# Kernel tuning notes

Hardware: AMD Instinct MI355X
Metric: run time of the kernel (lower is better)

Reference implementation:

```python
import jax, jax.numpy as jnp
import numpy as np

B, S, I, Q, H = 512, 196, 2048, 1024, 512


def _attn(X, g, wx, bx, wg, bg, wh, bh):
    # X: (B, S, F); g: (B, G) or None
    feat = jnp.einsum('bsf,fh->bsh', X, wx) + bx
    if g is not None:
        feat = feat + (g @ wg + bg)[:, None, :]
    h = jnp.tanh(feat)
    score = jnp.einsum('bsh,h->bs', h, wh) + bh  # (B, S)
    a = jax.nn.softmax(score, axis=1)
    return jnp.einsum('bs,bsf->bf', a, X)


def setup_inputs() -> dict:
    key = jax.random.key(0)
    ks = jax.random.split(key, 16)
    sc = lambda n: 1.0 / np.sqrt(n)
    d = {
        'ques_feat': jax.random.normal(ks[0], (B, Q), jnp.float32),
        'img_feat': jax.random.normal(ks[1], (B, S, I), jnp.float32),
        # attn1: X=ques (Q), no guidance
        'w1x': jax.random.uniform(ks[2], (Q, H), jnp.float32, -sc(Q), sc(Q)),
        'b1x': jnp.zeros((H,), jnp.float32),
        'w1h': jax.random.uniform(ks[3], (H,), jnp.float32, -sc(H), sc(H)),
        'b1h': jnp.zeros((), jnp.float32),
        # attn2: X=img (I), guidance=ques (Q)
        'w2x': jax.random.uniform(ks[4], (I, H), jnp.float32, -sc(I), sc(I)),
        'b2x': jnp.zeros((H,), jnp.float32),
        'w2g': jax.random.uniform(ks[5], (Q, H), jnp.float32, -sc(Q), sc(Q)),
        'b2g': jnp.zeros((H,), jnp.float32),
        'w2h': jax.random.uniform(ks[6], (H,), jnp.float32, -sc(H), sc(H)),
        'b2h': jnp.zeros((), jnp.float32),
        # attn3: X=ques (Q), guidance=img-attended (I)
        'w3x': jax.random.uniform(ks[7], (Q, H), jnp.float32, -sc(Q), sc(Q)),
        'b3x': jnp.zeros((H,), jnp.float32),
        'w3g': jax.random.uniform(ks[8], (I, H), jnp.float32, -sc(I), sc(I)),
        'b3g': jnp.zeros((H,), jnp.float32),
        'w3h': jax.random.uniform(ks[9], (H,), jnp.float32, -sc(H), sc(H)),
        'b3h': jnp.zeros((), jnp.float32),
    }
    return d


def reference(ques_feat, img_feat, w1x, b1x, w1h, b1h, w2x, b2x, w2g, b2g,
              w2h, b2h, w3x, b3x, w3g, b3g, w3h, b3h):
    q = ques_feat[:, None, :]  # (B, 1, Q)
    ques_self = _attn(q, None, w1x, b1x, None, None, w1h, b1h)          # (B, Q)
    img_attn = _attn(img_feat, ques_self, w2x, b2x, w2g, b2g, w2h, b2h)  # (B, I)
    ques_attn = _attn(q, img_attn, w3x, b3x, w3g, b3g, w3h, b3h)         # (B, Q)
    return (ques_attn, img_attn)
```

## Files before the change

kernel.cpp:

```cpp
#include <hip/hip_runtime.h>
#include <hip/hip_bf16.h>
#include <cstdint>


typedef __attribute__((ext_vector_type(8))) short bf16x8;
typedef __attribute__((ext_vector_type(4))) float f32x4;

typedef __attribute__((address_space(1))) const unsigned int as1_uint;
typedef __attribute__((address_space(3))) unsigned int as3_uint;

__device__ inline unsigned short f2bf(float f) {
    union { float f; unsigned u; } v; v.f = f;
    unsigned u = v.u;
    u += 0x7FFFu + ((u >> 16) & 1u);
    return (unsigned short)(u >> 16);
}

__device__ inline unsigned pk2(float lo, float hi) {
    __hip_bfloat162 h = __float22bfloat162_rn(make_float2(lo, hi));
    return *reinterpret_cast<unsigned*>(&h);
}

__device__ inline bf16x8 cvt8(uint4 lo, uint4 hi) {
    union { uint4 q; float f[4]; } a, b; a.q = lo; b.q = hi;
    union { unsigned u[4]; bf16x8 v; } r;
    r.u[0] = pk2(a.f[0], a.f[1]); r.u[1] = pk2(a.f[2], a.f[3]);
    r.u[2] = pk2(b.f[0], b.f[1]); r.u[3] = pk2(b.f[2], b.f[3]);
    return r.v;
}

__global__ void k_copy(const float* __restrict__ src, float* __restrict__ dst) {
    int i = blockIdx.x * blockDim.x + threadIdx.x;
    reinterpret_cast<float4*>(dst)[i] = reinterpret_cast<const float4*>(src)[i];
}

__global__ void k_pack_w(const float* __restrict__ w, unsigned short* __restrict__ wtf) {
    int kblk = blockIdx.x >> 5;
    int nblk = blockIdx.x & 31;
    int t = threadIdx.x;
    int kc8 = t >> 4, col = t & 15;
    const float* src = w + (size_t)(kblk * 64 + kc8 * 8) * 512 + nblk * 16 + col;
    unsigned short* dst = wtf + (size_t)(kblk * 32 + nblk) * 1024 + kc8 * 128 + col * 8;
    unsigned short tmp[8];
    #pragma unroll
    for (int j = 0; j < 8; ++j) tmp[j] = f2bf(src[(size_t)j * 512]);
    *reinterpret_cast<uint4*>(dst) = *reinterpret_cast<const uint4*>(tmp);
}

__global__ void k_cconst(const float* __restrict__ qf, const float* __restrict__ w2g,
                         const float* __restrict__ b2g, const float* __restrict__ b2x,
                         float* __restrict__ cc) {
    __shared__ float qls[2][1024];
    int b0 = blockIdx.x * 2;
    int t = threadIdx.x;
    #pragma unroll
    for (int j = 0; j < 2; ++j) {
        int idx = j * 256 + t;
        int bb = idx >> 8, c4 = idx & 255;
        float4 v = reinterpret_cast<const float4*>(qf + (size_t)(b0 + bb) * 1024)[c4];
        qls[bb][c4 * 4 + 0] = v.x; qls[bb][c4 * 4 + 1] = v.y;
        qls[bb][c4 * 4 + 2] = v.z; qls[bb][c4 * 4 + 3] = v.w;
    }
    __syncthreads();
    float a00 = 0.f, a01 = 0.f, a10 = 0.f, a11 = 0.f;
    #pragma unroll 8
    for (int q = 0; q < 1024; ++q) {
        float w0 = w2g[q * 512 + t];
        float w1 = w2g[q * 512 + 256 + t];
        float q0 = qls[0][q], q1 = qls[1][q];
        a00 += q0 * w0; a01 += q0 * w1;
        a10 += q1 * w0; a11 += q1 * w1;
    }
    float c0 = b2g[t] + b2x[t];
    float c1 = b2g[t + 256] + b2x[t + 256];
    cc[(size_t)b0 * 512 + t] = a00 + c0;
    cc[(size_t)b0 * 512 + t + 256] = a01 + c1;
    cc[(size_t)(b0 + 1) * 512 + t] = a10 + c0;
    cc[(size_t)(b0 + 1) * 512 + t + 256] = a11 + c1;
}

#define NSTEP 32

__global__ __launch_bounds__(512, 4) void k_scores(
    const float* __restrict__ X, const unsigned short* __restrict__ WTf,
    const float* __restrict__ cc, const float* __restrict__ w2h,
    float* __restrict__ scores)
{
    __shared__ __align__(16) char Ab[4][16384];
    __shared__ float slds[64];

    int tid = threadIdx.x;
    int wave = tid >> 6, lane = tid & 63;
    int l15 = lane & 15, l4 = lane >> 4;
    int r0 = blockIdx.x * 64;

    int srow = tid >> 4, spc = tid & 15;
    const char* xsrc = reinterpret_cast<const char*>(X + (size_t)(r0 + srow) * 2048)
                       + ((spc ^ (srow & 15)) << 4);
    const char* xsrc2 = xsrc + (size_t)32 * 8192;
    char* ldsw = &Ab[0][0] + wave * 1024;

    const unsigned short* wb0 = WTf + (size_t)wave * 4096 + l4 * 128 + l15 * 8;

    const char* abase = &Ab[0][0];
    int off00 = l15 * 256 + (((l4 * 2 + 0) ^ l15) << 4);
    int off01 = l15 * 256 + (((l4 * 2 + 1) ^ l15) << 4);
    int off10 = l15 * 256 + (((8 + l4 * 2 + 0) ^ l15) << 4);
    int off11 = l15 * 256 + (((8 + l4 * 2 + 1) ^ l15) << 4);

    if (tid < 64) slds[tid] = 0.0f;

    f32x4 acc[4][4];
    #pragma unroll
    for (int m = 0; m < 4; ++m)
        #pragma unroll
        for (int n = 0; n < 4; ++n) acc[m][n] = (f32x4){0.f, 0.f, 0.f, 0.f};

    bf16x8 brA[4], brB[4];

    #define GLOAD2(bufofs, step) do { \
        __builtin_amdgcn_global_load_lds((as1_uint*)(xsrc + (step) * 256), \
            (as3_uint*)(ldsw + (bufofs)), 16, 0, 2); \
        __builtin_amdgcn_global_load_lds((as1_uint*)(xsrc2 + (step) * 256), \
            (as3_uint*)(ldsw + (bufofs) + 8192), 16, 0, 2); } while (0)

    #define BLOAD(dst, t, kh) do { \
        const unsigned short* bp = wb0 + (size_t)(t) * 32768 + (kh) * 512; \
        dst[0] = *reinterpret_cast<const bf16x8*>(bp); \
        dst[1] = *reinterpret_cast<const bf16x8*>(bp + 1024); \
        dst[2] = *reinterpret_cast<const bf16x8*>(bp + 2048); \
        dst[3] = *reinterpret_cast<const bf16x8*>(bp + 3072); } while (0)

    #define MF(br, bufofs, offL, offH) do { \
        __builtin_amdgcn_s_setprio(1); \
        _Pragma("unroll") \
        for (int m = 0; m < 4; ++m) { \
            uint4 lo = *reinterpret_cast<const uint4*>(abase + (bufofs) + m * 4096 + (offL)); \
            uint4 hi = *reinterpret_cast<const uint4*>(abase + (bufofs) + m * 4096 + (offH)); \
            bf16x8 af = cvt8(lo, hi); \
            _Pragma("unroll") \
            for (int n = 0; n < 4; ++n) \
                acc[m][n] = __builtin_amdgcn_mfma_f32_16x16x32_bf16(af, br[n], acc[m][n], 0, 0, 0); \
        } \
        __builtin_amdgcn_s_setprio(0); } while (0)

    #define SBAR __builtin_amdgcn_sched_barrier(0)

    GLOAD2(0, 0);
    GLOAD2(16384, 1);
    GLOAD2(32768, 2);
    BLOAD(brA, 0, 0);
    asm volatile("s_waitcnt vmcnt(12)" ::: "memory");
    __builtin_amdgcn_s_barrier();

    #pragma unroll 1
    for (int t = 0; t < NSTEP; ++t) {
        int bufofs = (t & 3) * 16384;
        BLOAD(brB, t, 1);
        MF(brA, bufofs, off00, off01);
        if (t + 1 < NSTEP) BLOAD(brA, t + 1, 0);
        MF(brB, bufofs, off10, off11);
        SBAR;
        if (t + 3 < NSTEP) GLOAD2(((t + 3) & 3) * 16384, t + 3);
        SBAR;
        __builtin_amdgcn_s_barrier();
    }

    asm volatile("" ::: "memory");

    int b0 = r0 / 196;
    int sbreak = (b0 + 1) * 196 - r0;
    int b1 = b0 + 1; if (b1 > 511) b1 = 511;
    float cch0[4], cch1[4], whv[4];
    #pragma unroll
    for (int n = 0; n < 4; ++n) {
        int h = wave * 64 + n * 16 + l15;
        cch0[n] = cc[(size_t)b0 * 512 + h];
        cch1[n] = cc[(size_t)b1 * 512 + h];
        whv[n] = w2h[h];
    }
    #pragma unroll
    for (int m = 0; m < 4; ++m) {
        #pragma unroll
        for (int i = 0; i < 4; ++i) {
            int row = m * 16 + l4 * 4 + i;
            float p = 0.0f;
            #pragma unroll
            for (int n = 0; n < 4; ++n) {
                float x = acc[m][n][i] + ((row < sbreak) ? cch0[n] : cch1[n]);
                float th = 1.0f - 2.0f / (__expf(2.0f * x) + 1.0f);
                p += th * whv[n];
            }
            p += __shfl_xor(p, 1);
            p += __shfl_xor(p, 2);
            p += __shfl_xor(p, 4);
            p += __shfl_xor(p, 8);
            if (l15 == 0) atomicAdd(&slds[row], p);
        }
    }
    __syncthreads();
    if (tid < 64) scores[(size_t)r0 + tid] = slds[tid];
}

__global__ void k_softmax(float* sc) {
    int b = blockIdx.x, t = threadIdx.x;
    __shared__ float red[8];
    float v = (t < 196) ? sc[(size_t)b * 196 + t] : -3.0e38f;
    float m = v;
    for (int o = 32; o > 0; o >>= 1) m = fmaxf(m, __shfl_xor(m, o));
    if ((t & 63) == 0) red[t >> 6] = m;
    __syncthreads();
    m = fmaxf(fmaxf(red[0], red[1]), fmaxf(red[2], red[3]));
    float e = (t < 196) ? __expf(v - m) : 0.0f;
    float s = e;
    for (int o = 32; o > 0; o >>= 1) s += __shfl_xor(s, o);
    if ((t & 63) == 0) red[4 + (t >> 6)] = s;
    __syncthreads();
    float tot = red[4] + red[5] + red[6] + red[7];
    if (t < 196) sc[(size_t)b * 196 + t] = e / tot;
}

__global__ void k_wsum(const float* __restrict__ X, const float* __restrict__ a,
                       float* __restrict__ out1) {
    __shared__ float als[196];
    int b = blockIdx.x >> 1;
    int fh = (blockIdx.x & 1) * 1024;
    int t = threadIdx.x;
    if (t < 196) als[t] = a[(size_t)b * 196 + t];
    __syncthreads();
    int f = fh + t * 4;
    const float* Xb = X + (size_t)b * 196 * 2048 + f;
    float4 acc = {0.f, 0.f, 0.f, 0.f};
    #pragma unroll 4
    for (int s = 0; s < 196; ++s) {
        float4 x = *reinterpret_cast<const float4*>(Xb + (size_t)s * 2048);
        float w = als[s];
        acc.x += w * x.x; acc.y += w * x.y; acc.z += w * x.z; acc.w += w * x.w;
    }
    *reinterpret_cast<float4*>(out1 + (size_t)b * 2048 + f) = acc;
}

extern "C" void kernel_launch(void* const* d_in, const int* in_sizes, int n_in,
                              void* d_out, int out_size, void* d_ws, size_t ws_size,
                              hipStream_t stream) {
    const float* qf  = (const float*)d_in[0];
    const float* X   = (const float*)d_in[1];
    const float* w2x = (const float*)d_in[6];
    const float* b2x = (const float*)d_in[7];
    const float* w2g = (const float*)d_in[8];
    const float* b2g = (const float*)d_in[9];
    const float* w2h = (const float*)d_in[10];

    float* out0 = (float*)d_out;
    float* out1 = out0 + 512 * 1024;

    unsigned short* WTf = (unsigned short*)d_ws;
    float* cc = (float*)((char*)d_ws + (size_t)(2u << 20));
    float* sc = (float*)((char*)d_ws + (size_t)(3u << 20));

    k_copy<<<512, 256, 0, stream>>>(qf, out0);
    k_pack_w<<<1024, 128, 0, stream>>>(w2x, WTf);
    k_cconst<<<256, 256, 0, stream>>>(qf, w2g, b2g, b2x, cc);
    k_scores<<<1568, 512, 0, stream>>>(X, WTf, cc, w2h, sc);
    k_softmax<<<512, 256, 0, stream>>>(sc);
    k_wsum<<<1024, 256, 0, stream>>>(X, sc, out1);
}
```

Before: 531.1 us.

## Widen score K-tile and emit bf16 X copy for weighted sum

```diff
diff --git a/kernel.cpp b/kernel.cpp
--- a/kernel.cpp
+++ b/kernel.cpp
@@ -21,12 +21,23 @@
     return *reinterpret_cast<unsigned*>(&h);
 }
 
+__device__ inline unsigned pkq(unsigned a, unsigned b) {
+    union { unsigned u; float f; } x, y; x.u = a; y.u = b;
+    return pk2(x.f, y.f);
+}
+
 __device__ inline bf16x8 cvt8(uint4 lo, uint4 hi) {
-    union { uint4 q; float f[4]; } a, b; a.q = lo; b.q = hi;
     union { unsigned u[4]; bf16x8 v; } r;
-    r.u[0] = pk2(a.f[0], a.f[1]); r.u[1] = pk2(a.f[2], a.f[3]);
-    r.u[2] = pk2(b.f[0], b.f[1]); r.u[3] = pk2(b.f[2], b.f[3]);
+    r.u[0] = pkq(lo.x, lo.y); r.u[1] = pkq(lo.z, lo.w);
+    r.u[2] = pkq(hi.x, hi.y); r.u[3] = pkq(hi.z, hi.w);
     return r.v;
+}
+
+__device__ inline float bfhi(unsigned u) {
+    union { unsigned u; float f; } v; v.u = u & 0xFFFF0000u; return v.f;
+}
+__device__ inline float bflo(unsigned u) {
+    union { unsigned u; float f; } v; v.u = u << 16; return v.f;
 }
 
 __global__ void k_copy(const float* __restrict__ src, float* __restrict__ dst) {
@@ -79,14 +90,15 @@
     cc[(size_t)(b0 + 1) * 512 + t + 256] = a11 + c1;
 }
 
-#define NSTEP 32
-
-__global__ __launch_bounds__(512, 4) void k_scores(
+#define NSTEP 16
+
+template<int DOX>
+__global__ __launch_bounds__(512, 2) void k_scores_t(
     const float* __restrict__ X, const unsigned short* __restrict__ WTf,
     const float* __restrict__ cc, const float* __restrict__ w2h,
-    float* __restrict__ scores)
+    float* __restrict__ scores, unsigned short* __restrict__ xbf)
 {
-    __shared__ __align__(16) char Ab[4][16384];
+    __shared__ __align__(16) char Ab[4][32768];
     __shared__ float slds[64];
 
     int tid = threadIdx.x;
@@ -94,19 +106,25 @@
     int l15 = lane & 15, l4 = lane >> 4;
     int r0 = blockIdx.x * 64;
 
-    int srow = tid >> 4, spc = tid & 15;
-    const char* xsrc = reinterpret_cast<const char*>(X + (size_t)(r0 + srow) * 2048)
-                       + ((spc ^ (srow & 15)) << 4);
-    const char* xsrc2 = xsrc + (size_t)32 * 8192;
+    int srow = tid >> 5;
+    int spc = tid & 31;
+    int g0 = (spc ^ srow) << 4;
+    int g1 = (spc ^ (srow + 16)) << 4;
+    const char* xs0 = reinterpret_cast<const char*>(X + (size_t)(r0 + srow) * 2048) + g0;
+    const char* xs1 = reinterpret_cast<const char*>(X + (size_t)(r0 + srow + 16) * 2048) + g1;
+    const char* xs2 = reinterpret_cast<const char*>(X + (size_t)(r0 + srow + 32) * 2048) + g0;
+    const char* xs3 = reinterpret_cast<const char*>(X + (size_t)(r0 + srow + 48) * 2048) + g1;
     char* ldsw = &Ab[0][0] + wave * 1024;
 
     const unsigned short* wb0 = WTf + (size_t)wave * 4096 + l4 * 128 + l15 * 8;
 
     const char* abase = &Ab[0][0];
-    int off00 = l15 * 256 + (((l4 * 2 + 0) ^ l15) << 4);
-    int off01 = l15 * 256 + (((l4 * 2 + 1) ^ l15) << 4);
-    int off10 = l15 * 256 + (((8 + l4 * 2 + 0) ^ l15) << 4);
-    int off11 = l15 * 256 + (((8 + l4 * 2 + 1) ^ l15) << 4);
+    int q0v = ((l4 * 2 + 0) ^ l15) << 4;
+    int q1v = ((l4 * 2 + 1) ^ l15) << 4;
+    int voff0 = l15 * 512 + q0v;
+    int voff1 = l15 * 512 + q1v;
+
+    char* xd = reinterpret_cast<char*>(xbf) + (size_t)blockIdx.x * 262144 + tid * 32;
 
     if (tid < 64) slds[tid] = 0.0f;
 
@@ -116,27 +134,31 @@
         #pragma unroll
         for (int n = 0; n < 4; ++n) acc[m][n] = (f32x4){0.f, 0.f, 0.f, 0.f};
 
-    bf16x8 brA[4], brB[4];
-
-    #define GLOAD2(bufofs, step) do { \
-        __builtin_amdgcn_global_load_lds((as1_uint*)(xsrc + (step) * 256), \
-            (as3_uint*)(ldsw + (bufofs)), 16, 0, 2); \
-        __builtin_amdgcn_global_load_lds((as1_uint*)(xsrc2 + (step) * 256), \
-            (as3_uint*)(ldsw + (bufofs) + 8192), 16, 0, 2); } while (0)
+    bf16x8 brA[4], brB[4], brC[4];
+
+    #define GLL(src, dst) __builtin_amdgcn_global_load_lds( \
+        (as1_uint*)(src), (as3_uint*)(dst), 16, 0, 2)
+
+    #define GLOAD4(bufofs, step) do { \
+        GLL(xs0 + (size_t)(step) * 512, ldsw + (bufofs)); \
+        GLL(xs1 + (size_t)(step) * 512, ldsw + (bufofs) + 8192); \
+        GLL(xs2 + (size_t)(step) * 512, ldsw + (bufofs) + 16384); \
+        GLL(xs3 + (size_t)(step) * 512, ldsw + (bufofs) + 24576); } while (0)
 
     #define BLOAD(dst, t, kh) do { \
-        const unsigned short* bp = wb0 + (size_t)(t) * 32768 + (kh) * 512; \
+        const unsigned short* bp = wb0 + (size_t)(2 * (t) + ((kh) >> 1)) * 32768 + ((kh) & 1) * 512; \
         dst[0] = *reinterpret_cast<const bf16x8*>(bp); \
         dst[1] = *reinterpret_cast<const bf16x8*>(bp + 1024); \
         dst[2] = *reinterpret_cast<const bf16x8*>(bp + 2048); \
         dst[3] = *reinterpret_cast<const bf16x8*>(bp + 3072); } while (0)
 
-    #define MF(br, bufofs, offL, offH) do { \
+    #define MF(br, bufofs, kh) do { \
         __builtin_amdgcn_s_setprio(1); \
         _Pragma("unroll") \
         for (int m = 0; m < 4; ++m) { \
-            uint4 lo = *reinterpret_cast<const uint4*>(abase + (bufofs) + m * 4096 + (offL)); \
-            uint4 hi = *reinterpret_cast<const uint4*>(abase + (bufofs) + m * 4096 + (offH)); \
+            int cst = ((kh) * 128) ^ ((m & 1) * 256); \
+            uint4 lo = *reinterpret_cast<const uint4*>(abase + (bufofs) + m * 8192 + (voff0 ^ cst)); \
+            uint4 hi = *reinterpret_cast<const uint4*>(abase + (bufofs) + m * 8192 + (voff1 ^ cst)); \
             bf16x8 af = cvt8(lo, hi); \
             _Pragma("unroll") \
             for (int n = 0; n < 4; ++n) \
@@ -144,27 +166,44 @@
         } \
         __builtin_amdgcn_s_setprio(0); } while (0)
 
-    #define SBAR __builtin_amdgcn_sched_barrier(0)
-
-    GLOAD2(0, 0);
-    GLOAD2(16384, 1);
-    GLOAD2(32768, 2);
+    #define STORE_TILE(bufofs, t) do { if (DOX) { \
+        const uint4* sp = reinterpret_cast<const uint4*>(abase + (bufofs) + tid * 64); \
+        uint4 s0 = sp[0], s1 = sp[1], s2 = sp[2], s3 = sp[3]; \
+        uint4 o0, o1; \
+        o0.x = pkq(s0.x, s0.y); o0.y = pkq(s0.z, s0.w); \
+        o0.z = pkq(s1.x, s1.y); o0.w = pkq(s1.z, s1.w); \
+        o1.x = pkq(s2.x, s2.y); o1.y = pkq(s2.z, s2.w); \
+        o1.z = pkq(s3.x, s3.y); o1.w = pkq(s3.z, s3.w); \
+        *reinterpret_cast<uint4*>(xd + (size_t)(t) * 16384) = o0; \
+        *reinterpret_cast<uint4*>(xd + (size_t)(t) * 16384 + 16) = o1; } } while (0)
+
+    #define STEP(T, SA, SB, SC, LAST) do { \
+        const int bo_ = ((T) & 3) * 32768; \
+        if ((T) + 3 < NSTEP) GLOAD4((((T) + 3) & 3) * 32768, (T) + 3); \
+        MF(SA, bo_, 0); BLOAD(SA, (T), 3); \
+        MF(SB, bo_, 1); if (!(LAST)) BLOAD(SB, (T) + 1, 0); \
+        MF(SC, bo_, 2); if (!(LAST)) BLOAD(SC, (T) + 1, 1); \
+        MF(SA, bo_, 3); if (!(LAST)) BLOAD(SA, (T) + 1, 2); \
+        STORE_TILE(bo_, T); \
+        __builtin_amdgcn_sched_barrier(0); \
+        __builtin_amdgcn_s_barrier(); } while (0)
+
+    GLOAD4(0, 0);
+    GLOAD4(32768, 1);
+    GLOAD4(65536, 2);
     BLOAD(brA, 0, 0);
-    asm volatile("s_waitcnt vmcnt(12)" ::: "memory");
+    BLOAD(brB, 0, 1);
+    BLOAD(brC, 0, 2);
+    asm volatile("s_waitcnt vmcnt(20)" ::: "memory");
     __builtin_amdgcn_s_barrier();
 
     #pragma unroll 1
-    for (int t = 0; t < NSTEP; ++t) {
-        int bufofs = (t & 3) * 16384;
-        BLOAD(brB, t, 1);
-        MF(brA, bufofs, off00, off01);
-        if (t + 1 < NSTEP) BLOAD(brA, t + 1, 0);
-        MF(brB, bufofs, off10, off11);
-        SBAR;
-        if (t + 3 < NSTEP) GLOAD2(((t + 3) & 3) * 16384, t + 3);
-        SBAR;
-        __builtin_amdgcn_s_barrier();
-    }
+    for (int T = 0; T < 15; T += 3) {
+        STEP(T,     brA, brB, brC, 0);
+        STEP(T + 1, brB, brC, brA, 0);
+        STEP(T + 2, brC, brA, brB, 0);
+    }
+    STEP(15, brA, brB, brC, 1);
 
     asm volatile("" ::: "memory");
 
@@ -220,6 +259,36 @@
     if (t < 196) sc[(size_t)b * 196 + t] = e / tot;
 }
 
+__global__ __launch_bounds__(256) void k_wsum_bf(const unsigned short* __restrict__ Xbf,
+                                                 const float* __restrict__ a,
+                                                 float* __restrict__ out1) {
+    __shared__ float als[196];
+    int b = blockIdx.x >> 1;
+    int half = blockIdx.x & 1;
+    int t = threadIdx.x;
+    if (t < 196) als[t] = a[(size_t)b * 196 + t];
+    __syncthreads();
+    int f = half * 1024 + t * 4;
+    int cg = f >> 2;
+    int step = cg >> 5;
+    int gcolin = cg & 31;
+    const char* xb = reinterpret_cast<const char*>(Xbf);
+    float a0 = 0.f, a1 = 0.f, a2 = 0.f, a3 = 0.f;
+    int r = b * 196;
+    #pragma unroll 4
+    for (int s = 0; s < 196; ++s, ++r) {
+        int tile = r >> 6, row = r & 63;
+        size_t byte = (size_t)tile * 262144 + (size_t)step * 16384
+                      + (size_t)(row * 32 + (gcolin ^ (row & 31))) * 8;
+        uint2 v = *reinterpret_cast<const uint2*>(xb + byte);
+        float w = als[s];
+        a0 += w * bflo(v.x); a1 += w * bfhi(v.x);
+        a2 += w * bflo(v.y); a3 += w * bfhi(v.y);
+    }
+    float4 o = {a0, a1, a2, a3};
+    *reinterpret_cast<float4*>(out1 + (size_t)b * 2048 + f) = o;
+}
+
 __global__ void k_wsum(const float* __restrict__ X, const float* __restrict__ a,
                        float* __restrict__ out1) {
     __shared__ float als[196];
@@ -257,11 +326,20 @@
     unsigned short* WTf = (unsigned short*)d_ws;
     float* cc = (float*)((char*)d_ws + (size_t)(2u << 20));
     float* sc = (float*)((char*)d_ws + (size_t)(3u << 20));
+    unsigned short* xbf = (unsigned short*)((char*)d_ws + (size_t)(4u << 20));
+    const size_t XBF_BYTES = (size_t)1568 * 262144;
+    int big = (ws_size >= (size_t)(4u << 20) + XBF_BYTES) ? 1 : 0;
 
     k_copy<<<512, 256, 0, stream>>>(qf, out0);
     k_pack_w<<<1024, 128, 0, stream>>>(w2x, WTf);
     k_cconst<<<256, 256, 0, stream>>>(qf, w2g, b2g, b2x, cc);
-    k_scores<<<1568, 512, 0, stream>>>(X, WTf, cc, w2h, sc);
-    k_softmax<<<512, 256, 0, stream>>>(sc);
-    k_wsum<<<1024, 256, 0, stream>>>(X, sc, out1);
-}
+    if (big) {
+        k_scores_t<1><<<1568, 512, 0, stream>>>(X, WTf, cc, w2h, sc, xbf);
+        k_softmax<<<512, 256, 0, stream>>>(sc);
+        k_wsum_bf<<<1024, 256, 0, stream>>>(xbf, sc, out1);
+    } else {
+        k_scores_t<0><<<1568, 512, 0, stream>>>(X, WTf, cc, w2h, sc, xbf);
+        k_softmax<<<512, 256, 0, stream>>>(sc);
+        k_wsum<<<1024, 256, 0, stream>>>(X, sc, out1);
+    }
+}
```

New measurement: 553.3 us. 1.04x slower.

## Emit bf16 copy of image tiles from scoring kernel for weighted sum

Applied to the files above, without the earlier changes.

```diff
diff --git a/kernel.cpp b/kernel.cpp
--- a/kernel.cpp
+++ b/kernel.cpp
@@ -21,12 +21,23 @@
     return *reinterpret_cast<unsigned*>(&h);
 }
 
+__device__ inline unsigned pkq(unsigned a, unsigned b) {
+    union { unsigned u; float f; } x, y; x.u = a; y.u = b;
+    return pk2(x.f, y.f);
+}
+
 __device__ inline bf16x8 cvt8(uint4 lo, uint4 hi) {
-    union { uint4 q; float f[4]; } a, b; a.q = lo; b.q = hi;
     union { unsigned u[4]; bf16x8 v; } r;
-    r.u[0] = pk2(a.f[0], a.f[1]); r.u[1] = pk2(a.f[2], a.f[3]);
-    r.u[2] = pk2(b.f[0], b.f[1]); r.u[3] = pk2(b.f[2], b.f[3]);
+    r.u[0] = pkq(lo.x, lo.y); r.u[1] = pkq(lo.z, lo.w);
+    r.u[2] = pkq(hi.x, hi.y); r.u[3] = pkq(hi.z, hi.w);
     return r.v;
+}
+
+__device__ inline float bfhi(unsigned u) {
+    union { unsigned u; float f; } v; v.u = u & 0xFFFF0000u; return v.f;
+}
+__device__ inline float bflo(unsigned u) {
+    union { unsigned u; float f; } v; v.u = u << 16; return v.f;
 }
 
 __global__ void k_copy(const float* __restrict__ src, float* __restrict__ dst) {
@@ -81,10 +92,11 @@
 
 #define NSTEP 32
 
-__global__ __launch_bounds__(512, 4) void k_scores(
+template<int DOX>
+__global__ __launch_bounds__(512, 4) void k_scores_t(
     const float* __restrict__ X, const unsigned short* __restrict__ WTf,
     const float* __restrict__ cc, const float* __restrict__ w2h,
-    float* __restrict__ scores)
+    float* __restrict__ scores, unsigned short* __restrict__ xbf)
 {
     __shared__ __align__(16) char Ab[4][16384];
     __shared__ float slds[64];
@@ -107,6 +119,8 @@
     int off01 = l15 * 256 + (((l4 * 2 + 1) ^ l15) << 4);
     int off10 = l15 * 256 + (((8 + l4 * 2 + 0) ^ l15) << 4);
     int off11 = l15 * 256 + (((8 + l4 * 2 + 1) ^ l15) << 4);
+
+    char* xd = reinterpret_cast<char*>(xbf) + (size_t)blockIdx.x * 262144 + tid * 16;
 
     if (tid < 64) slds[tid] = 0.0f;
 
@@ -144,13 +158,21 @@
         } \
         __builtin_amdgcn_s_setprio(0); } while (0)
 
+    #define STORE_TILE(bufofs, t) do { if (DOX) { \
+        const uint4* sp = reinterpret_cast<const uint4*>(abase + (bufofs) + tid * 32); \
+        uint4 s0 = sp[0], s1 = sp[1]; \
+        uint4 o; \
+        o.x = pkq(s0.x, s0.y); o.y = pkq(s0.z, s0.w); \
+        o.z = pkq(s1.x, s1.y); o.w = pkq(s1.z, s1.w); \
+        *reinterpret_cast<uint4*>(xd + (size_t)(t) * 8192) = o; } } while (0)
+
     #define SBAR __builtin_amdgcn_sched_barrier(0)
 
     GLOAD2(0, 0);
     GLOAD2(16384, 1);
     GLOAD2(32768, 2);
     BLOAD(brA, 0, 0);
-    asm volatile("s_waitcnt vmcnt(12)" ::: "memory");
+    asm volatile("s_waitcnt vmcnt(8)" ::: "memory");
     __builtin_amdgcn_s_barrier();
 
     #pragma unroll 1
@@ -160,6 +182,7 @@
         MF(brA, bufofs, off00, off01);
         if (t + 1 < NSTEP) BLOAD(brA, t + 1, 0);
         MF(brB, bufofs, off10, off11);
+        STORE_TILE(bufofs, t);
         SBAR;
         if (t + 3 < NSTEP) GLOAD2(((t + 3) & 3) * 16384, t + 3);
         SBAR;
@@ -220,6 +243,36 @@
     if (t < 196) sc[(size_t)b * 196 + t] = e / tot;
 }
 
+__global__ __launch_bounds__(256) void k_wsum_bf(const unsigned short* __restrict__ Xbf,
+                                                 const float* __restrict__ a,
+                                                 float* __restrict__ out1) {
+    __shared__ float als[196];
+    int b = blockIdx.x >> 1;
+    int half = blockIdx.x & 1;
+    int t = threadIdx.x;
+    if (t < 196) als[t] = a[(size_t)b * 196 + t];
+    __syncthreads();
+    int f = half * 1024 + t * 4;
+    int step = f >> 6;
+    int gcol = (f & 63) >> 2;
+    const char* xb = reinterpret_cast<const char*>(Xbf);
+    float a0 = 0.f, a1 = 0.f, a2 = 0.f, a3 = 0.f;
+    int r = b * 196;
+    #pragma unroll 4
+    for (int s = 0; s < 196; ++s, ++r) {
+        int tile = r >> 6, row = r & 63;
+        int pc = gcol ^ (row & 15);
+        size_t byte = (size_t)tile * 262144 + (size_t)step * 8192
+                      + (size_t)(row * 16 + pc) * 8;
+        uint2 v = *reinterpret_cast<const uint2*>(xb + byte);
+        float w = als[s];
+        a0 += w * bflo(v.x); a1 += w * bfhi(v.x);
+        a2 += w * bflo(v.y); a3 += w * bfhi(v.y);
+    }
+    float4 o = {a0, a1, a2, a3};
+    *reinterpret_cast<float4*>(out1 + (size_t)b * 2048 + f) = o;
+}
+
 __global__ void k_wsum(const float* __restrict__ X, const float* __restrict__ a,
                        float* __restrict__ out1) {
     __shared__ float als[196];
@@ -257,11 +310,20 @@
     unsigned short* WTf = (unsigned short*)d_ws;
     float* cc = (float*)((char*)d_ws + (size_t)(2u << 20));
     float* sc = (float*)((char*)d_ws + (size_t)(3u << 20));
+    unsigned short* xbf = (unsigned short*)((char*)d_ws + (size_t)(4u << 20));
+    const size_t XBF_BYTES = (size_t)1568 * 262144;
+    int big = (ws_size >= (size_t)(4u << 20) + XBF_BYTES) ? 1 : 0;
 
     k_copy<<<512, 256, 0, stream>>>(qf, out0);
     k_pack_w<<<1024, 128, 0, stream>>>(w2x, WTf);
     k_cconst<<<256, 256, 0, stream>>>(qf, w2g, b2g, b2x, cc);
-    k_scores<<<1568, 512, 0, stream>>>(X, WTf, cc, w2h, sc);
-    k_softmax<<<512, 256, 0, stream>>>(sc);
-    k_wsum<<<1024, 256, 0, stream>>>(X, sc, out1);
-}
+    if (big) {
+        k_scores_t<1><<<1568, 512, 0, stream>>>(X, WTf, cc, w2h, sc, xbf);
+        k_softmax<<<512, 256, 0, stream>>>(sc);
+        k_wsum_bf<<<1024, 256, 0, stream>>>(xbf, sc, out1);
+    } else {
+        k_scores_t<0><<<1568, 512, 0, stream>>>(X, WTf, cc, w2h, sc, xbf);
+        k_softmax<<<512, 256, 0, stream>>>(sc);
+        k_wsum<<<1024, 256, 0, stream>>>(X, sc, out1);
+    }
+}
```

New measurement: 550.1 us. 1.04x slower.

## Split score GEMM across two H-halves with 256-thread blocks and deeper B prefetch

Applied to the files above, without the earlier changes.

```diff
diff --git a/kernel.cpp b/kernel.cpp
--- a/kernel.cpp
+++ b/kernel.cpp
@@ -21,11 +21,15 @@
     return *reinterpret_cast<unsigned*>(&h);
 }
 
+__device__ inline unsigned pkq(unsigned a, unsigned b) {
+    union { unsigned u; float f; } x, y; x.u = a; y.u = b;
+    return pk2(x.f, y.f);
+}
+
 __device__ inline bf16x8 cvt8(uint4 lo, uint4 hi) {
-    union { uint4 q; float f[4]; } a, b; a.q = lo; b.q = hi;
     union { unsigned u[4]; bf16x8 v; } r;
-    r.u[0] = pk2(a.f[0], a.f[1]); r.u[1] = pk2(a.f[2], a.f[3]);
-    r.u[2] = pk2(b.f[0], b.f[1]); r.u[3] = pk2(b.f[2], b.f[3]);
+    r.u[0] = pkq(lo.x, lo.y); r.u[1] = pkq(lo.z, lo.w);
+    r.u[2] = pkq(hi.x, hi.y); r.u[3] = pkq(hi.z, hi.w);
     return r.v;
 }
 
@@ -81,10 +85,10 @@
 
 #define NSTEP 32
 
-__global__ __launch_bounds__(512, 4) void k_scores(
+__global__ __launch_bounds__(256, 2) void k_scores(
     const float* __restrict__ X, const unsigned short* __restrict__ WTf,
     const float* __restrict__ cc, const float* __restrict__ w2h,
-    float* __restrict__ scores)
+    float* __restrict__ sc0, float* __restrict__ sc1)
 {
     __shared__ __align__(16) char Ab[4][16384];
     __shared__ float slds[64];
@@ -92,15 +96,23 @@
     int tid = threadIdx.x;
     int wave = tid >> 6, lane = tid & 63;
     int l15 = lane & 15, l4 = lane >> 4;
-    int r0 = blockIdx.x * 64;
-
-    int srow = tid >> 4, spc = tid & 15;
-    const char* xsrc = reinterpret_cast<const char*>(X + (size_t)(r0 + srow) * 2048)
-                       + ((spc ^ (srow & 15)) << 4);
-    const char* xsrc2 = xsrc + (size_t)32 * 8192;
+
+    int bi = blockIdx.x;
+    int tile = (bi >> 4) * 8 + (bi & 7);
+    int half = (bi >> 3) & 1;
+    int r0 = tile * 64;
+
+    int sr = tid >> 4;
+    int spc = tid & 15;
+    int gswz = (spc ^ sr) << 4;
+    const char* xs0 = reinterpret_cast<const char*>(X + (size_t)(r0 + sr) * 2048) + gswz;
+    const char* xs1 = reinterpret_cast<const char*>(X + (size_t)(r0 + 16 + sr) * 2048) + gswz;
+    const char* xs2 = reinterpret_cast<const char*>(X + (size_t)(r0 + 32 + sr) * 2048) + gswz;
+    const char* xs3 = reinterpret_cast<const char*>(X + (size_t)(r0 + 48 + sr) * 2048) + gswz;
     char* ldsw = &Ab[0][0] + wave * 1024;
 
-    const unsigned short* wb0 = WTf + (size_t)wave * 4096 + l4 * 128 + l15 * 8;
+    const unsigned short* wb0 = WTf + (size_t)(half * 16 + wave * 4) * 1024
+                                + l4 * 128 + l15 * 8;
 
     const char* abase = &Ab[0][0];
     int off00 = l15 * 256 + (((l4 * 2 + 0) ^ l15) << 4);
@@ -116,22 +128,29 @@
         #pragma unroll
         for (int n = 0; n < 4; ++n) acc[m][n] = (f32x4){0.f, 0.f, 0.f, 0.f};
 
-    bf16x8 brA[4], brB[4];
-
-    #define GLOAD2(bufofs, step) do { \
-        __builtin_amdgcn_global_load_lds((as1_uint*)(xsrc + (step) * 256), \
-            (as3_uint*)(ldsw + (bufofs)), 16, 0, 2); \
-        __builtin_amdgcn_global_load_lds((as1_uint*)(xsrc2 + (step) * 256), \
-            (as3_uint*)(ldsw + (bufofs) + 8192), 16, 0, 2); } while (0)
-
-    #define BLOAD(dst, t, kh) do { \
-        const unsigned short* bp = wb0 + (size_t)(t) * 32768 + (kh) * 512; \
+    bf16x8 b0[8], b1[8], b2[8];
+
+    #define GLL(src, dst) __builtin_amdgcn_global_load_lds( \
+        (as1_uint*)(src), (as3_uint*)(dst), 16, 0, 0)
+
+    #define GLOAD4(bufofs, step) do { \
+        GLL(xs0 + (size_t)(step) * 256, ldsw + (bufofs)); \
+        GLL(xs1 + (size_t)(step) * 256, ldsw + (bufofs) + 4096); \
+        GLL(xs2 + (size_t)(step) * 256, ldsw + (bufofs) + 8192); \
+        GLL(xs3 + (size_t)(step) * 256, ldsw + (bufofs) + 12288); } while (0)
+
+    #define BLOAD8(dst, t) do { \
+        const unsigned short* bp = wb0 + (size_t)(t) * 32768; \
         dst[0] = *reinterpret_cast<const bf16x8*>(bp); \
         dst[1] = *reinterpret_cast<const bf16x8*>(bp + 1024); \
         dst[2] = *reinterpret_cast<const bf16x8*>(bp + 2048); \
-        dst[3] = *reinterpret_cast<const bf16x8*>(bp + 3072); } while (0)
-
-    #define MF(br, bufofs, offL, offH) do { \
+        dst[3] = *reinterpret_cast<const bf16x8*>(bp + 3072); \
+        dst[4] = *reinterpret_cast<const bf16x8*>(bp + 512); \
+        dst[5] = *reinterpret_cast<const bf16x8*>(bp + 1536); \
+        dst[6] = *reinterpret_cast<const bf16x8*>(bp + 2560); \
+        dst[7] = *reinterpret_cast<const bf16x8*>(bp + 3584); } while (0)
+
+    #define MF(brp, bufofs, offL, offH) do { \
         __builtin_amdgcn_s_setprio(1); \
         _Pragma("unroll") \
         for (int m = 0; m < 4; ++m) { \
@@ -140,43 +159,50 @@
             bf16x8 af = cvt8(lo, hi); \
             _Pragma("unroll") \
             for (int n = 0; n < 4; ++n) \
-                acc[m][n] = __builtin_amdgcn_mfma_f32_16x16x32_bf16(af, br[n], acc[m][n], 0, 0, 0); \
+                acc[m][n] = __builtin_amdgcn_mfma_f32_16x16x32_bf16(af, (brp)[n], acc[m][n], 0, 0, 0); \
         } \
         __builtin_amdgcn_s_setprio(0); } while (0)
 
     #define SBAR __builtin_amdgcn_sched_barrier(0)
 
-    GLOAD2(0, 0);
-    GLOAD2(16384, 1);
-    GLOAD2(32768, 2);
-    BLOAD(brA, 0, 0);
-    asm volatile("s_waitcnt vmcnt(12)" ::: "memory");
+    #define STEP(T, CUR, NXT) do { \
+        const int bo_ = ((T) & 3) * 16384; \
+        if ((T) + 3 < NSTEP) GLOAD4((((T) + 3) & 3) * 16384, (T) + 3); \
+        if ((T) + 2 < NSTEP) BLOAD8(NXT, (T) + 2); \
+        SBAR; \
+        MF((CUR), bo_, off00, off01); \
+        MF((CUR) + 4, bo_, off10, off11); \
+        SBAR; \
+        __builtin_amdgcn_s_barrier(); } while (0)
+
+    GLOAD4(0, 0);
+    GLOAD4(16384, 1);
+    GLOAD4(32768, 2);
+    BLOAD8(b0, 0);
+    BLOAD8(b1, 1);
+    asm volatile("s_waitcnt vmcnt(24)" ::: "memory");
     __builtin_amdgcn_s_barrier();
 
     #pragma unroll 1
-    for (int t = 0; t < NSTEP; ++t) {
-        int bufofs = (t & 3) * 16384;
-        BLOAD(brB, t, 1);
-        MF(brA, bufofs, off00, off01);
-        if (t + 1 < NSTEP) BLOAD(brA, t + 1, 0);
-        MF(brB, bufofs, off10, off11);
-        SBAR;
-        if (t + 3 < NSTEP) GLOAD2(((t + 3) & 3) * 16384, t + 3);
-        SBAR;
-        __builtin_amdgcn_s_barrier();
-    }
+    for (int T = 0; T < 30; T += 3) {
+        STEP(T,     b0, b2);
+        STEP(T + 1, b1, b0);
+        STEP(T + 2, b2, b1);
+    }
+    STEP(30, b0, b2);
+    STEP(31, b1, b0);
 
     asm volatile("" ::: "memory");
 
-    int b0 = r0 / 196;
-    int sbreak = (b0 + 1) * 196 - r0;
-    int b1 = b0 + 1; if (b1 > 511) b1 = 511;
+    int b0r = r0 / 196;
+    int sbreak = (b0r + 1) * 196 - r0;
+    int b1r = b0r + 1; if (b1r > 511) b1r = 511;
     float cch0[4], cch1[4], whv[4];
     #pragma unroll
     for (int n = 0; n < 4; ++n) {
-        int h = wave * 64 + n * 16 + l15;
-        cch0[n] = cc[(size_t)b0 * 512 + h];
-        cch1[n] = cc[(size_t)b1 * 512 + h];
+        int h = half * 256 + wave * 64 + n * 16 + l15;
+        cch0[n] = cc[(size_t)b0r * 512 + h];
+        cch1[n] = cc[(size_t)b1r * 512 + h];
         whv[n] = w2h[h];
     }
     #pragma unroll
@@ -199,13 +225,18 @@
         }
     }
     __syncthreads();
-    if (tid < 64) scores[(size_t)r0 + tid] = slds[tid];
-}
-
-__global__ void k_softmax(float* sc) {
+    if (tid < 64) {
+        float* dst = half ? sc1 : sc0;
+        dst[(size_t)r0 + tid] = slds[tid];
+    }
+}
+
+__global__ void k_softmax(const float* __restrict__ sc0, const float* __restrict__ sc1,
+                          float* __restrict__ a) {
     int b = blockIdx.x, t = threadIdx.x;
     __shared__ float red[8];
-    float v = (t < 196) ? sc[(size_t)b * 196 + t] : -3.0e38f;
+    float v = -3.0e38f;
+    if (t < 196) v = sc0[(size_t)b * 196 + t] + sc1[(size_t)b * 196 + t];
     float m = v;
     for (int o = 32; o > 0; o >>= 1) m = fmaxf(m, __shfl_xor(m, o));
     if ((t & 63) == 0) red[t >> 6] = m;
@@ -217,7 +248,7 @@
     if ((t & 63) == 0) red[4 + (t >> 6)] = s;
     __syncthreads();
     float tot = red[4] + red[5] + red[6] + red[7];
-    if (t < 196) sc[(size_t)b * 196 + t] = e / tot;
+    if (t < 196) a[(size_t)b * 196 + t] = e / tot;
 }
 
 __global__ void k_wsum(const float* __restrict__ X, const float* __restrict__ a,
@@ -255,13 +286,15 @@
     float* out1 = out0 + 512 * 1024;
 
     unsigned short* WTf = (unsigned short*)d_ws;
-    float* cc = (float*)((char*)d_ws + (size_t)(2u << 20));
-    float* sc = (float*)((char*)d_ws + (size_t)(3u << 20));
+    float* cc  = (float*)((char*)d_ws + (size_t)(2u << 20));
+    float* sc0 = (float*)((char*)d_ws + (size_t)(3u << 20));
+    float* sc1 = (float*)((char*)d_ws + (size_t)(3u << 20) + (512u << 10));
+    float* aw  = (float*)((char*)d_ws + (size_t)(4u << 20));
 
     k_copy<<<512, 256, 0, stream>>>(qf, out0);
     k_pack_w<<<1024, 128, 0, stream>>>(w2x, WTf);
     k_cconst<<<256, 256, 0, stream>>>(qf, w2g, b2g, b2x, cc);
-    k_scores<<<1568, 512, 0, stream>>>(X, WTf, cc, w2h, sc);
-    k_softmax<<<512, 256, 0, stream>>>(sc);
-    k_wsum<<<1024, 256, 0, stream>>>(X, sc, out1);
-}
+    k_scores<<<3136, 256, 0, stream>>>(X, WTf, cc, w2h, sc0, sc1);
+    k_softmax<<<512, 256, 0, stream>>>(sc0, sc1, aw);
+    k_wsum<<<1024, 256, 0, stream>>>(X, aw, out1);
+}
```

Measured after the change: 604.6 us. 13.8% more time.
